# Optimization experiments

Measured on AMD Instinct MI355X. Metric: run time of the kernel, lower is better.

## Reference

```python
import jax, jax.numpy as jnp
import numpy as np

B, S, D = 2, 2048, 1024
H, HD = 16, 64  # num heads, head dim
EPS = 1e-12
SCALING = HD ** -0.5


def rotate_half(x):
    x1, x2 = jnp.split(x, 2, axis=-1)
    return jnp.concatenate([-x2, x1], axis=-1)


def setup_inputs() -> dict:
    key = jax.random.key(0)
    ks = jax.random.split(key, 12)
    hidden_states = jax.random.normal(ks[0], (B, S, D), dtype=jnp.float32)
    # RoPE tables (standard rotate-half convention)
    inv_freq = 1.0 / (10000.0 ** (np.arange(0, HD, 2, dtype=np.float32) / HD))
    pos = np.arange(S, dtype=np.float32)
    freqs = np.outer(pos, inv_freq)  # [S, HD/2]
    emb = np.concatenate([freqs, freqs], axis=-1)  # [S, HD]
    cos = jnp.asarray(np.cos(emb))
    sin = jnp.asarray(np.sin(emb))
    w = 0.02
    return {
        "hidden_states": hidden_states,
        "cos": cos,
        "sin": sin,
        "Wq": jax.random.normal(ks[1], (D, D), dtype=jnp.float32) * w,
        "bq": jnp.zeros((D,), dtype=jnp.float32),
        "Wk": jax.random.normal(ks[2], (D, D), dtype=jnp.float32) * w,
        "bk": jnp.zeros((D,), dtype=jnp.float32),
        "Wv": jax.random.normal(ks[3], (D, D), dtype=jnp.float32) * w,
        "bv": jnp.zeros((D,), dtype=jnp.float32),
        "Wo": jax.random.normal(ks[4], (D, D), dtype=jnp.float32) * w,
        "bo": jnp.zeros((D,), dtype=jnp.float32),
        "ln_w": jnp.ones((D,), dtype=jnp.float32),
        "ln_b": jnp.zeros((D,), dtype=jnp.float32),
    }


def reference(hidden_states, cos, sin, Wq, bq, Wk, bk, Wv, bv, Wo, bo, ln_w, ln_b):
    b, s, d = hidden_states.shape
    # QKV projections -> [b, h, s, hd]
    def proj(W, bias):
        return (hidden_states @ W.T + bias).reshape(b, s, H, HD).transpose(0, 2, 1, 3)
    q, k, v = proj(Wq, bq), proj(Wk, bk), proj(Wv, bv)
    # RoPE (cos/sin broadcast over batch and head dims)
    c = cos[None, None, :, :]
    sn = sin[None, None, :, :]
    q = q * c + rotate_half(q) * sn
    k = k * c + rotate_half(k) * sn
    # Faithful to source: query pre-scaled AND scaling applied inside attention
    q = q * SCALING
    scores = jnp.einsum("bhsd,bhtd->bhst", q, k) * SCALING
    attn = jax.nn.softmax(scores, axis=-1)
    ctx = jnp.einsum("bhst,bhtd->bhsd", attn, v)  # [b,h,s,hd]
    ctx = ctx.transpose(0, 2, 1, 3).reshape(b, s, d)
    # output dense + residual + LayerNorm
    out = ctx @ Wo.T + bo + hidden_states
    mu = jnp.mean(out, axis=-1, keepdims=True)
    var = jnp.var(out, axis=-1, keepdims=True)
    return (out - mu) / jnp.sqrt(var + EPS) * ln_w + ln_b
```

## Files before the change

kernel.cpp:

```cpp
#include <hip/hip_runtime.h>
#include <hip/hip_bf16.h>
#include <stdint.h>


typedef unsigned short ushort_t;
typedef short bf16x8 __attribute__((ext_vector_type(8)));
typedef float f32x4 __attribute__((ext_vector_type(4)));
typedef float f32x16 __attribute__((ext_vector_type(16)));
typedef unsigned short ushort8 __attribute__((ext_vector_type(8)));

#define LOG2E 1.4426950408889634f

__device__ __forceinline__ ushort_t f2b(float f) {
  uint32_t x = __builtin_bit_cast(uint32_t, f);
  return (ushort_t)((x + 0x7FFFu + ((x >> 16) & 1u)) >> 16);
}

__device__ __forceinline__ float b2f(ushort_t u) {
  return __builtin_bit_cast(float, (uint32_t)u << 16);
}

__device__ __forceinline__ uint32_t cvt_pk_bf16(float lo, float hi) {
  uint32_t r;
  asm("v_cvt_pk_bf16_f32 %0, %1, %2" : "=v"(r) : "v"(lo), "v"(hi));
  return r;
}

__device__ __forceinline__ void permswap(uint32_t& a, uint32_t& b) {
  asm volatile("v_permlane32_swap_b32 %0, %1" : "+v"(a), "+v"(b));
}

__device__ __forceinline__ void gload16(const void* gptr, void* ldsptr) {
  __builtin_amdgcn_global_load_lds(
      (const __attribute__((address_space(1))) uint32_t*)gptr,
      (__attribute__((address_space(3))) uint32_t*)ldsptr, 16, 0, 0);
}

__global__ void cast_all_kernel(const float* __restrict__ h,
                                const float* __restrict__ a, const float* __restrict__ b,
                                const float* __restrict__ c, const float* __restrict__ d2,
                                ushort_t* __restrict__ oh, ushort_t* __restrict__ oa,
                                ushort_t* __restrict__ ob, ushort_t* __restrict__ oc,
                                ushort_t* __restrict__ od) {
  const int blk = blockIdx.x;
  const float* src;
  ushort_t* dst;
  int rel;
  if (blk < 2048) { src = h; dst = oh; rel = blk; }
  else {
    const int w = (blk - 2048) >> 9;
    rel = (blk - 2048) & 511;
    src = w == 0 ? a : w == 1 ? b : w == 2 ? c : d2;
    dst = w == 0 ? oa : w == 1 ? ob : w == 2 ? oc : od;
  }
  const int i = (rel * 256 + threadIdx.x) * 8;
  const float4* s = (const float4*)(src + i);
  float4 x = s[0], y = s[1];
  ushort8 o = { f2b(x.x), f2b(x.y), f2b(x.z), f2b(x.w),
                f2b(y.x), f2b(y.y), f2b(y.z), f2b(y.w) };
  *(ushort8*)(dst + i) = o;
}

__global__ __launch_bounds__(256) void gemm_qkv(
    const ushort_t* __restrict__ hid, const ushort_t* __restrict__ wq,
    const ushort_t* __restrict__ wk, const ushort_t* __restrict__ wv,
    const float* __restrict__ bq, const float* __restrict__ bk,
    const float* __restrict__ bv, const float* __restrict__ cosT,
    const float* __restrict__ sinT, ushort_t* __restrict__ qout,
    ushort_t* __restrict__ kout, ushort_t* __restrict__ vtout)
{
  constexpr int K = 1024;
  __shared__ uint4 SB[3072];
  const int which = blockIdx.z;
  const ushort_t* A;
  const ushort_t* Bm;
  const float* bias;
  int m0, n0;
  if (which == 0)      { A = hid; Bm = wq; bias = bq; m0 = blockIdx.x * 128; n0 = blockIdx.y * 128; }
  else if (which == 1) { A = hid; Bm = wk; bias = bk; m0 = blockIdx.x * 128; n0 = blockIdx.y * 128; }
  else                 { A = wv;  Bm = hid; bias = bv; m0 = blockIdx.y * 128; n0 = blockIdx.x * 128; }

  const int tid = threadIdx.x;
  const int wave = tid >> 6, lane = tid & 63;
  const int d = lane & 15, g = lane >> 4;
  const int wm = (wave >> 1) * 64, wn = (wave & 1) * 64;

  const ushort_t* ag = A + (size_t)(m0 + (tid >> 2)) * K + (tid & 3) * 8;
  const ushort_t* bg = Bm + (size_t)(n0 + (tid >> 2)) * K + (tid & 3) * 8;

  f32x4 acc[4][4] = {};

#define STAGE_Q(buf, k0)                                           \
  {                                                                \
    char* dst = (char*)SB + (buf) * 16384 + wave * 1024;           \
    gload16(ag + (k0), dst);                                       \
    gload16(ag + 64 * K + (k0), dst + 4096);                       \
    gload16(bg + (k0), dst + 8192);                                \
    gload16(bg + 64 * K + (k0), dst + 12288);                      \
  }

#define COMPUTE_Q(buf)                                                          \
  {                                                                             \
    bf16x8 af[4], bfr[4];                                                       \
    _Pragma("unroll") for (int i = 0; i < 4; ++i)                               \
        af[i] = __builtin_bit_cast(bf16x8,                                      \
            SB[(buf) * 1024 + (wm + i * 16 + d) * 4 + g]);                      \
    _Pragma("unroll") for (int j = 0; j < 4; ++j)                               \
        bfr[j] = __builtin_bit_cast(bf16x8,                                     \
            SB[(buf) * 1024 + 512 + (wn + j * 16 + d) * 4 + g]);                \
    _Pragma("unroll") for (int i = 0; i < 4; ++i)                               \
        _Pragma("unroll") for (int j = 0; j < 4; ++j)                           \
            acc[i][j] = __builtin_amdgcn_mfma_f32_16x16x32_bf16(                \
                af[i], bfr[j], acc[i][j], 0, 0, 0);                             \
  }

  STAGE_Q(0, 0);
  STAGE_Q(1, 32);
  asm volatile("s_waitcnt vmcnt(4)" ::: "memory");
  __builtin_amdgcn_s_barrier();

  int bufc = 0;
  for (int t = 0; t < 30; ++t) {
    int bufn = bufc + 2; if (bufn >= 3) bufn -= 3;
    STAGE_Q(bufn, (t + 2) * 32);
    COMPUTE_Q(bufc);
    asm volatile("s_waitcnt vmcnt(4)" ::: "memory");
    __builtin_amdgcn_s_barrier();
    bufc = (bufc == 2) ? 0 : bufc + 1;
  }
  COMPUTE_Q(bufc);
  asm volatile("s_waitcnt vmcnt(0)" ::: "memory");
  __builtin_amdgcn_s_barrier();
  bufc = (bufc == 2) ? 0 : bufc + 1;
  COMPUTE_Q(bufc);
#undef STAGE_Q
#undef COMPUTE_Q

  if (which <= 1) {
    ushort_t* O = which == 0 ? qout : kout;
    const float qscale = which == 0 ? (LOG2E / 64.0f) : 1.0f;
    const int head_base = n0 + wn;
    const int h = head_base >> 6;
#pragma unroll
    for (int i = 0; i < 4; ++i) {
#pragma unroll
      for (int r = 0; r < 4; ++r) {
        const int m = m0 + wm + i * 16 + g * 4 + r;
        const int s = m & 2047, b = m >> 11;
#pragma unroll
        for (int j = 0; j < 4; ++j) {
          const int c = j * 16 + d;
          const float v0 = acc[i][j][r] + bias[head_base + c];
          const float v1 = acc[i][j ^ 2][r] + bias[head_base + (c ^ 32)];
          const float rot = (c < 32) ? -v1 : v1;
          const float vr = (v0 * cosT[s * 64 + c] + rot * sinT[s * 64 + c]) * qscale;
          O[(size_t)(((b << 4) + h) * 2048 + s) * 64 + c] = f2b(vr);
        }
      }
    }
  } else {
    ushort_t* O = vtout;
#pragma unroll
    for (int i = 0; i < 4; ++i) {
#pragma unroll
      for (int r = 0; r < 4; ++r) {
        const int fr = m0 + wm + i * 16 + g * 4 + r;
        const float bv2 = bias[fr];
        const int h = fr >> 6, dd = fr & 63;
#pragma unroll
        for (int j = 0; j < 4; ++j) {
          const int tok = n0 + wn + j * 16 + d;
          const int b = tok >> 11, s = tok & 2047;
          O[(size_t)(((b << 4) + h) * 64 + dd) * 2048 + s] = f2b(acc[i][j][r] + bv2);
        }
      }
    }
  }
}

__global__ __launch_bounds__(256) void gemm_wo(
    const ushort_t* __restrict__ A, const ushort_t* __restrict__ B,
    const float* __restrict__ bias, const float* __restrict__ resid,
    ushort_t* __restrict__ O)
{
  constexpr int K = 1024;
  __shared__ uint4 SB[3072];
  const int tid = threadIdx.x;
  const int wave = tid >> 6, lane = tid & 63;
  const int d = lane & 15, g = lane >> 4;
  const int m0 = blockIdx.x * 128, n0 = blockIdx.y * 128;
  const int wm = (wave >> 1) * 64, wn = (wave & 1) * 64;

  const ushort_t* ag = A + (size_t)(m0 + (tid >> 2)) * K + (tid & 3) * 8;
  const ushort_t* bg = B + (size_t)(n0 + (tid >> 2)) * K + (tid & 3) * 8;

  f32x4 acc[4][4] = {};

#define STAGE_W(buf, k0)                                           \
  {                                                                \
    char* dst = (char*)SB + (buf) * 16384 + wave * 1024;           \
    gload16(ag + (k0), dst);                                       \
    gload16(ag + 64 * K + (k0), dst + 4096);                       \
    gload16(bg + (k0), dst + 8192);                                \
    gload16(bg + 64 * K + (k0), dst + 12288);                      \
  }

#define COMPUTE_W(buf)                                                          \
  {                                                                             \
    bf16x8 af[4], bfr[4];                                                       \
    _Pragma("unroll") for (int i = 0; i < 4; ++i)                               \
        af[i] = __builtin_bit_cast(bf16x8,                                      \
            SB[(buf) * 1024 + (wm + i * 16 + d) * 4 + g]);                      \
    _Pragma("unroll") for (int j = 0; j < 4; ++j)                               \
        bfr[j] = __builtin_bit_cast(bf16x8,                                     \
            SB[(buf) * 1024 + 512 + (wn + j * 16 + d) * 4 + g]);                \
    _Pragma("unroll") for (int i = 0; i < 4; ++i)                               \
        _Pragma("unroll") for (int j = 0; j < 4; ++j)                           \
            acc[i][j] = __builtin_amdgcn_mfma_f32_16x16x32_bf16(                \
                af[i], bfr[j], acc[i][j], 0, 0, 0);                             \
  }

  STAGE_W(0, 0);
  STAGE_W(1, 32);
  asm volatile("s_waitcnt vmcnt(4)" ::: "memory");
  __builtin_amdgcn_s_barrier();

  int bufc = 0;
  for (int t = 0; t < 30; ++t) {
    int bufn = bufc + 2; if (bufn >= 3) bufn -= 3;
    STAGE_W(bufn, (t + 2) * 32);
    COMPUTE_W(bufc);
    asm volatile("s_waitcnt vmcnt(4)" ::: "memory");
    __builtin_amdgcn_s_barrier();
    bufc = (bufc == 2) ? 0 : bufc + 1;
  }
  COMPUTE_W(bufc);
  asm volatile("s_waitcnt vmcnt(0)" ::: "memory");
  __builtin_amdgcn_s_barrier();
  bufc = (bufc == 2) ? 0 : bufc + 1;
  COMPUTE_W(bufc);
#undef STAGE_W
#undef COMPUTE_W

#pragma unroll
  for (int i = 0; i < 4; ++i)
#pragma unroll
    for (int r = 0; r < 4; ++r) {
      const int m = m0 + wm + i * 16 + g * 4 + r;
#pragma unroll
      for (int j = 0; j < 4; ++j) {
        const int n = n0 + wn + j * 16 + d;
        O[(size_t)m * 1024 + n] =
            f2b(acc[i][j][r] + bias[n] + resid[(size_t)m * 1024 + n]);
      }
    }
}

__global__ __launch_bounds__(512) void attn_kernel(
    const ushort_t* __restrict__ Q, const ushort_t* __restrict__ Kb,
    const ushort_t* __restrict__ VT, ushort_t* __restrict__ ctx)
{
  __shared__ uint4 KV[2048];
  __shared__ float Ls[256];
  const int orig = blockIdx.x;
  const int wgid = (orig & 7) * 64 + (orig >> 3);
  const int bh = wgid >> 4;
  const int q0 = (wgid & 15) * 128;
  const int tid = threadIdx.x;
  const int wave = tid >> 6, lane = tid & 63;
  const int qw = wave >> 1, half = wave & 1;
  const int ql = lane & 31, h2 = lane >> 5;
  const int qrow = q0 + qw * 32 + ql;

  bf16x8 qf[4];
  {
    const ushort_t* qp = Q + ((size_t)bh * 2048 + qrow) * 64 + h2 * 8;
#pragma unroll
    for (int s = 0; s < 4; ++s)
      qf[s] = __builtin_bit_cast(bf16x8, *(const uint4*)(qp + 16 * s));
  }

  bf16x8 onesf;
  {
    uint4 ou = {0x3F803F80u, 0x3F803F80u, 0x3F803F80u, 0x3F803F80u};
    onesf = __builtin_bit_cast(bf16x8, ou);
  }

  const int st_row = tid >> 3, st_c8 = tid & 7;
  const ushort_t* kgp = Kb + (size_t)(bh * 2048 + st_row) * 64 + st_c8 * 8;
  const ushort_t* vgp = VT + (size_t)(bh * 64 + st_row) * 2048 + st_c8 * 8;
  const int sidx = st_row * 8 + (st_c8 ^ (st_row & 7));

  uint4 kr = *(const uint4*)(kgp);
  uint4 vr = *(const uint4*)(vgp);
  KV[sidx] = kr;
  KV[512 + sidx] = vr;
  __syncthreads();

  f32x16 cacc[2] = {};
  f32x16 lacc = {};

#define ATT_COMPUTE(CB)                                                         \
  {                                                                             \
    f32x16 z = {};                                                              \
    _Pragma("unroll") for (int s = 0; s < 4; ++s) {                             \
      bf16x8 kf = __builtin_bit_cast(bf16x8,                                    \
          KV[(CB) + (half * 32 + ql) * 8 + ((2 * s + h2) ^ (ql & 7))]);         \
      z = __builtin_amdgcn_mfma_f32_32x32x16_bf16(kf, qf[s], z, 0, 0, 0);       \
    }                                                                           \
    bf16x8 pf[2];                                                               \
    _Pragma("unroll") for (int s2 = 0; s2 < 2; ++s2) {                          \
      const int rb = s2 * 8;                                                    \
      float p0 = __builtin_amdgcn_exp2f(z[rb + 0]);                             \
      float p1 = __builtin_amdgcn_exp2f(z[rb + 1]);                             \
      float p2 = __builtin_amdgcn_exp2f(z[rb + 2]);                             \
      float p3 = __builtin_amdgcn_exp2f(z[rb + 3]);                             \
      float p4 = __builtin_amdgcn_exp2f(z[rb + 4]);                             \
      float p5 = __builtin_amdgcn_exp2f(z[rb + 5]);                             \
      float p6 = __builtin_amdgcn_exp2f(z[rb + 6]);                             \
      float p7 = __builtin_amdgcn_exp2f(z[rb + 7]);                             \
      uint32_t a1 = cvt_pk_bf16(p0, p1);                                        \
      uint32_t a2 = cvt_pk_bf16(p2, p3);                                        \
      uint32_t b1 = cvt_pk_bf16(p4, p5);                                        \
      uint32_t b2 = cvt_pk_bf16(p6, p7);                                        \
      permswap(a1, b1);                                                         \
      permswap(a2, b2);                                                         \
      uint4 u = {a1, a2, b1, b2};                                               \
      pf[s2] = __builtin_bit_cast(bf16x8, u);                                   \
    }                                                                           \
    _Pragma("unroll") for (int s2 = 0; s2 < 2; ++s2)                            \
      lacc = __builtin_amdgcn_mfma_f32_32x32x16_bf16(onesf, pf[s2], lacc,       \
                                                     0, 0, 0);                  \
    _Pragma("unroll") for (int dt = 0; dt < 2; ++dt)                            \
      _Pragma("unroll") for (int s2 = 0; s2 < 2; ++s2) {                        \
        const int s = 2 * half + s2;                                            \
        bf16x8 vf = __builtin_bit_cast(bf16x8,                                  \
            KV[(CB) + 512 + (dt * 32 + ql) * 8 + ((2 * s + h2) ^ (ql & 7))]);   \
        cacc[dt] = __builtin_amdgcn_mfma_f32_32x32x16_bf16(vf, pf[s2],          \
                                                           cacc[dt], 0, 0, 0); \
      }                                                                         \
  }

  const ushort_t* kP = kgp + 4096;
  const ushort_t* vP = vgp + 64;
  for (int tt = 0; tt < 16; ++tt) {
    kr = *(const uint4*)(kP);
    vr = *(const uint4*)(vP);
    ATT_COMPUTE(0)
    KV[1024 + sidx] = kr;
    KV[1536 + sidx] = vr;
    __syncthreads();
    if (tt < 15) {
      kr = *(const uint4*)(kP + 4096);
      vr = *(const uint4*)(vP + 64);
    }
    ATT_COMPUTE(1024)
    if (tt < 15) {
      KV[sidx] = kr;
      KV[512 + sidx] = vr;
      __syncthreads();
    }
    kP += 8192;
    vP += 128;
  }
#undef ATT_COMPUTE

  float lsum = lacc[0];

  __syncthreads();
  float* Lf = (float*)KV;
  const int slot = qw * 64 + lane;
  if (half == 1) {
#pragma unroll
    for (int dt = 0; dt < 2; ++dt)
#pragma unroll
      for (int r = 0; r < 16; ++r)
        Lf[slot * 32 + ((dt * 16 + r) ^ (lane & 31))] = cacc[dt][r];
    Ls[slot] = lsum;
  }
  __syncthreads();
  if (half == 0) {
#pragma unroll
    for (int dt = 0; dt < 2; ++dt)
#pragma unroll
      for (int r = 0; r < 16; ++r)
        cacc[dt][r] += Lf[slot * 32 + ((dt * 16 + r) ^ (lane & 31))];
    lsum += Ls[slot];

    const float rinv = 1.0f / lsum;
    const int b = bh >> 4, h = bh & 15;
    ushort_t* cp = ctx + ((size_t)(b * 2048 + qrow)) * 1024 + h * 64 + h2 * 4;
#pragma unroll
    for (int dt = 0; dt < 2; ++dt)
#pragma unroll
      for (int t = 0; t < 4; ++t) {
        uint2 w;
        w.x = cvt_pk_bf16(cacc[dt][4 * t + 0] * rinv, cacc[dt][4 * t + 1] * rinv);
        w.y = cvt_pk_bf16(cacc[dt][4 * t + 2] * rinv, cacc[dt][4 * t + 3] * rinv);
        *(uint2*)(cp + dt * 32 + t * 8) = w;
      }
  }
}

__global__ __launch_bounds__(256) void ln_kernel(const ushort_t* __restrict__ x,
    const float* __restrict__ w, const float* __restrict__ b2, float* __restrict__ out)
{
  const int row = blockIdx.x, tid = threadIdx.x;
  const uint2 u = ((const uint2*)(x + (size_t)row * 1024))[tid];
  float v0 = b2f((ushort_t)(u.x & 0xFFFF));
  float v1 = b2f((ushort_t)(u.x >> 16));
  float v2 = b2f((ushort_t)(u.y & 0xFFFF));
  float v3 = b2f((ushort_t)(u.y >> 16));
  float s = (v0 + v1) + (v2 + v3);
  float ss = (v0 * v0 + v1 * v1) + (v2 * v2 + v3 * v3);
#pragma unroll
  for (int off = 32; off > 0; off >>= 1) {
    s += __shfl_down(s, off, 64);
    ss += __shfl_down(ss, off, 64);
  }
  __shared__ float red[8];
  if ((tid & 63) == 0) { red[tid >> 6] = s; red[4 + (tid >> 6)] = ss; }
  __syncthreads();
  const float S = red[0] + red[1] + red[2] + red[3];
  const float SS = red[4] + red[5] + red[6] + red[7];
  const float mu = S * (1.f / 1024.f);
  const float rstd = rsqrtf(SS * (1.f / 1024.f) - mu * mu + 1e-12f);
  const int c = tid * 4;
  float4 o;
  o.x = (v0 - mu) * rstd * w[c + 0] + b2[c + 0];
  o.y = (v1 - mu) * rstd * w[c + 1] + b2[c + 1];
  o.z = (v2 - mu) * rstd * w[c + 2] + b2[c + 2];
  o.w = (v3 - mu) * rstd * w[c + 3] + b2[c + 3];
  ((float4*)(out + (size_t)row * 1024))[tid] = o;
}

extern "C" void kernel_launch(void* const* d_in, const int* in_sizes, int n_in,
                              void* d_out, int out_size, void* d_ws, size_t ws_size,
                              hipStream_t stream) {
  const float* hidden = (const float*)d_in[0];
  const float* cosT = (const float*)d_in[1];
  const float* sinT = (const float*)d_in[2];
  const float* Wq = (const float*)d_in[3];
  const float* bq = (const float*)d_in[4];
  const float* Wk = (const float*)d_in[5];
  const float* bk = (const float*)d_in[6];
  const float* Wv = (const float*)d_in[7];
  const float* bv = (const float*)d_in[8];
  const float* Wo = (const float*)d_in[9];
  const float* bo = (const float*)d_in[10];
  const float* lnw = (const float*)d_in[11];
  const float* lnb = (const float*)d_in[12];

  char* ws = (char*)d_ws;
  const size_t MB = 1u << 20;
  ushort_t* hid_bf = (ushort_t*)(ws);
  ushort_t* wq_bf = (ushort_t*)(ws + 8 * MB);
  ushort_t* wk_bf = (ushort_t*)(ws + 10 * MB);
  ushort_t* wv_bf = (ushort_t*)(ws + 12 * MB);
  ushort_t* wo_bf = (ushort_t*)(ws + 14 * MB);
  ushort_t* q_buf = (ushort_t*)(ws + 16 * MB);
  ushort_t* k_buf = (ushort_t*)(ws + 24 * MB);
  ushort_t* vt_buf = (ushort_t*)(ws + 32 * MB);
  ushort_t* ctx_bf = (ushort_t*)(ws + 40 * MB);
  ushort_t* out_pre = (ushort_t*)(ws + 16 * MB);

  cast_all_kernel<<<4096, 256, 0, stream>>>(hidden, Wq, Wk, Wv, Wo,
                                            hid_bf, wq_bf, wk_bf, wv_bf, wo_bf);

  gemm_qkv<<<dim3(32, 8, 3), 256, 0, stream>>>(hid_bf, wq_bf, wk_bf, wv_bf,
                                               bq, bk, bv, cosT, sinT,
                                               q_buf, k_buf, vt_buf);
  attn_kernel<<<512, 512, 0, stream>>>(q_buf, k_buf, vt_buf, ctx_bf);
  gemm_wo<<<dim3(32, 8), 256, 0, stream>>>(ctx_bf, wo_bf, bo, hidden, out_pre);
  ln_kernel<<<4096, 256, 0, stream>>>(out_pre, lnw, lnb, (float*)d_out);
}
```

Baseline: 108.2 us.

## Fuse Q and K projections in one block to share the hidden-state tile

Q/K blocks now load one hidden-state tile and multiply it against both Wq and Wk, keeping two accumulator sets. V keeps its own block path, and the grid shrinks from three z-slices to two. The goal is fewer global loads of the activations and shared RoPE table reads. The cost is more registers and LDS per block (72KB), which may cut occupancy, and uneven work between Q/K blocks and V blocks.

```diff
diff --git a/kernel.cpp b/kernel.cpp
--- a/kernel.cpp
+++ b/kernel.cpp
@@ -70,108 +70,169 @@
     ushort_t* __restrict__ kout, ushort_t* __restrict__ vtout)
 {
   constexpr int K = 1024;
-  __shared__ uint4 SB[3072];
-  const int which = blockIdx.z;
-  const ushort_t* A;
-  const ushort_t* Bm;
-  const float* bias;
-  int m0, n0;
-  if (which == 0)      { A = hid; Bm = wq; bias = bq; m0 = blockIdx.x * 128; n0 = blockIdx.y * 128; }
-  else if (which == 1) { A = hid; Bm = wk; bias = bk; m0 = blockIdx.x * 128; n0 = blockIdx.y * 128; }
-  else                 { A = wv;  Bm = hid; bias = bv; m0 = blockIdx.y * 128; n0 = blockIdx.x * 128; }
-
+  __shared__ uint4 SB[4608];
   const int tid = threadIdx.x;
   const int wave = tid >> 6, lane = tid & 63;
   const int d = lane & 15, g = lane >> 4;
   const int wm = (wave >> 1) * 64, wn = (wave & 1) * 64;
 
-  const ushort_t* ag = A + (size_t)(m0 + (tid >> 2)) * K + (tid & 3) * 8;
-  const ushort_t* bg = Bm + (size_t)(n0 + (tid >> 2)) * K + (tid & 3) * 8;
-
-  f32x4 acc[4][4] = {};
-
-#define STAGE_Q(buf, k0)                                           \
+  if (blockIdx.z == 0) {
+    const int m0 = blockIdx.x * 128, n0 = blockIdx.y * 128;
+    const ushort_t* ag = hid + (size_t)(m0 + (tid >> 2)) * K + (tid & 3) * 8;
+    const ushort_t* qg = wq + (size_t)(n0 + (tid >> 2)) * K + (tid & 3) * 8;
+    const ushort_t* kg = wk + (size_t)(n0 + (tid >> 2)) * K + (tid & 3) * 8;
+
+    f32x4 accq[4][4] = {};
+    f32x4 acck[4][4] = {};
+
+#define STAGE_QK(buf, k0)                                          \
   {                                                                \
-    char* dst = (char*)SB + (buf) * 16384 + wave * 1024;           \
-    gload16(ag + (k0), dst);                                       \
-    gload16(ag + 64 * K + (k0), dst + 4096);                       \
-    gload16(bg + (k0), dst + 8192);                                \
-    gload16(bg + 64 * K + (k0), dst + 12288);                      \
-  }
-
-#define COMPUTE_Q(buf)                                                          \
+    char* base = (char*)(SB + (buf) * 1536) + wave * 1024;         \
+    gload16(ag + (k0), base);                                      \
+    gload16(ag + 64 * K + (k0), base + 4096);                      \
+    gload16(qg + (k0), base + 8192);                               \
+    gload16(qg + 64 * K + (k0), base + 12288);                     \
+    gload16(kg + (k0), base + 16384);                              \
+    gload16(kg + 64 * K + (k0), base + 20480);                     \
+  }
+
+#define COMPUTE_QK(buf)                                                         \
+  {                                                                             \
+    bf16x8 af[4], bfq[4], bfk[4];                                               \
+    _Pragma("unroll") for (int i = 0; i < 4; ++i)                               \
+        af[i] = __builtin_bit_cast(bf16x8,                                      \
+            SB[(buf) * 1536 + (wm + i * 16 + d) * 4 + g]);                      \
+    _Pragma("unroll") for (int j = 0; j < 4; ++j) {                             \
+        bfq[j] = __builtin_bit_cast(bf16x8,                                     \
+            SB[(buf) * 1536 + 512 + (wn + j * 16 + d) * 4 + g]);                \
+        bfk[j] = __builtin_bit_cast(bf16x8,                                     \
+            SB[(buf) * 1536 + 1024 + (wn + j * 16 + d) * 4 + g]);               \
+    }                                                                           \
+    _Pragma("unroll") for (int i = 0; i < 4; ++i)                               \
+        _Pragma("unroll") for (int j = 0; j < 4; ++j) {                         \
+            accq[i][j] = __builtin_amdgcn_mfma_f32_16x16x32_bf16(               \
+                af[i], bfq[j], accq[i][j], 0, 0, 0);                            \
+            acck[i][j] = __builtin_amdgcn_mfma_f32_16x16x32_bf16(               \
+                af[i], bfk[j], acck[i][j], 0, 0, 0);                            \
+        }                                                                       \
+  }
+
+    STAGE_QK(0, 0);
+    STAGE_QK(1, 32);
+    asm volatile("s_waitcnt vmcnt(6)" ::: "memory");
+    __builtin_amdgcn_s_barrier();
+
+    int bufc = 0;
+    for (int t = 0; t < 30; ++t) {
+      int bufn = bufc + 2; if (bufn >= 3) bufn -= 3;
+      STAGE_QK(bufn, (t + 2) * 32);
+      COMPUTE_QK(bufc);
+      asm volatile("s_waitcnt vmcnt(6)" ::: "memory");
+      __builtin_amdgcn_s_barrier();
+      bufc = (bufc == 2) ? 0 : bufc + 1;
+    }
+    COMPUTE_QK(bufc);
+    asm volatile("s_waitcnt vmcnt(0)" ::: "memory");
+    __builtin_amdgcn_s_barrier();
+    bufc = (bufc == 2) ? 0 : bufc + 1;
+    COMPUTE_QK(bufc);
+#undef STAGE_QK
+#undef COMPUTE_QK
+
+    const int head_base = n0 + wn;
+    const int h = head_base >> 6;
+#pragma unroll
+    for (int i = 0; i < 4; ++i) {
+#pragma unroll
+      for (int r = 0; r < 4; ++r) {
+        const int m = m0 + wm + i * 16 + g * 4 + r;
+        const int s = m & 2047, b = m >> 11;
+        const size_t orow = (size_t)(((b << 4) + h) * 2048 + s) * 64;
+#pragma unroll
+        for (int j = 0; j < 4; ++j) {
+          const int c = j * 16 + d;
+          const float cs = cosT[s * 64 + c];
+          const float sn = sinT[s * 64 + c];
+          {
+            const float v0 = accq[i][j][r] + bq[head_base + c];
+            const float v1 = accq[i][j ^ 2][r] + bq[head_base + (c ^ 32)];
+            const float rot = (c < 32) ? -v1 : v1;
+            qout[orow + c] = f2b((v0 * cs + rot * sn) * (LOG2E / 64.0f));
+          }
+          {
+            const float v0 = acck[i][j][r] + bk[head_base + c];
+            const float v1 = acck[i][j ^ 2][r] + bk[head_base + (c ^ 32)];
+            const float rot = (c < 32) ? -v1 : v1;
+            kout[orow + c] = f2b(v0 * cs + rot * sn);
+          }
+        }
+      }
+    }
+  } else {
+    const int m0 = blockIdx.y * 128, n0 = blockIdx.x * 128;
+    const ushort_t* ag = wv + (size_t)(m0 + (tid >> 2)) * K + (tid & 3) * 8;
+    const ushort_t* bg = hid + (size_t)(n0 + (tid >> 2)) * K + (tid & 3) * 8;
+
+    f32x4 acc[4][4] = {};
+
+#define STAGE_V(buf, k0)                                           \
+  {                                                                \
+    char* base = (char*)(SB + (buf) * 1536) + wave * 1024;         \
+    gload16(ag + (k0), base);                                      \
+    gload16(ag + 64 * K + (k0), base + 4096);                      \
+    gload16(bg + (k0), base + 8192);                               \
+    gload16(bg + 64 * K + (k0), base + 12288);                     \
+  }
+
+#define COMPUTE_V(buf)                                                          \
   {                                                                             \
     bf16x8 af[4], bfr[4];                                                       \
     _Pragma("unroll") for (int i = 0; i < 4; ++i)                               \
         af[i] = __builtin_bit_cast(bf16x8,                                      \
-            SB[(buf) * 1024 + (wm + i * 16 + d) * 4 + g]);                      \
+            SB[(buf) * 1536 + (wm + i * 16 + d) * 4 + g]);                      \
     _Pragma("unroll") for (int j = 0; j < 4; ++j)                               \
         bfr[j] = __builtin_bit_cast(bf16x8,                                     \
-            SB[(buf) * 1024 + 512 + (wn + j * 16 + d) * 4 + g]);                \
+            SB[(buf) * 1536 + 512 + (wn + j * 16 + d) * 4 + g]);                \
     _Pragma("unroll") for (int i = 0; i < 4; ++i)                               \
         _Pragma("unroll") for (int j = 0; j < 4; ++j)                           \
             acc[i][j] = __builtin_amdgcn_mfma_f32_16x16x32_bf16(                \
                 af[i], bfr[j], acc[i][j], 0, 0, 0);                             \
   }
 
-  STAGE_Q(0, 0);
-  STAGE_Q(1, 32);
-  asm volatile("s_waitcnt vmcnt(4)" ::: "memory");
-  __builtin_amdgcn_s_barrier();
-
-  int bufc = 0;
-  for (int t = 0; t < 30; ++t) {
-    int bufn = bufc + 2; if (bufn >= 3) bufn -= 3;
-    STAGE_Q(bufn, (t + 2) * 32);
-    COMPUTE_Q(bufc);
+    STAGE_V(0, 0);
+    STAGE_V(1, 32);
     asm volatile("s_waitcnt vmcnt(4)" ::: "memory");
     __builtin_amdgcn_s_barrier();
+
+    int bufc = 0;
+    for (int t = 0; t < 30; ++t) {
+      int bufn = bufc + 2; if (bufn >= 3) bufn -= 3;
+      STAGE_V(bufn, (t + 2) * 32);
+      COMPUTE_V(bufc);
+      asm volatile("s_waitcnt vmcnt(4)" ::: "memory");
+      __builtin_amdgcn_s_barrier();
+      bufc = (bufc == 2) ? 0 : bufc + 1;
+    }
+    COMPUTE_V(bufc);
+    asm volatile("s_waitcnt vmcnt(0)" ::: "memory");
+    __builtin_amdgcn_s_barrier();
     bufc = (bufc == 2) ? 0 : bufc + 1;
-  }
-  COMPUTE_Q(bufc);
-  asm volatile("s_waitcnt vmcnt(0)" ::: "memory");
-  __builtin_amdgcn_s_barrier();
-  bufc = (bufc == 2) ? 0 : bufc + 1;
-  COMPUTE_Q(bufc);
-#undef STAGE_Q
-#undef COMPUTE_Q
-
-  if (which <= 1) {
-    ushort_t* O = which == 0 ? qout : kout;
-    const float qscale = which == 0 ? (LOG2E / 64.0f) : 1.0f;
-    const int head_base = n0 + wn;
-    const int h = head_base >> 6;
-#pragma unroll
-    for (int i = 0; i < 4; ++i) {
-#pragma unroll
-      for (int r = 0; r < 4; ++r) {
-        const int m = m0 + wm + i * 16 + g * 4 + r;
-        const int s = m & 2047, b = m >> 11;
-#pragma unroll
-        for (int j = 0; j < 4; ++j) {
-          const int c = j * 16 + d;
-          const float v0 = acc[i][j][r] + bias[head_base + c];
-          const float v1 = acc[i][j ^ 2][r] + bias[head_base + (c ^ 32)];
-          const float rot = (c < 32) ? -v1 : v1;
-          const float vr = (v0 * cosT[s * 64 + c] + rot * sinT[s * 64 + c]) * qscale;
-          O[(size_t)(((b << 4) + h) * 2048 + s) * 64 + c] = f2b(vr);
-        }
-      }
-    }
-  } else {
-    ushort_t* O = vtout;
+    COMPUTE_V(bufc);
+#undef STAGE_V
+#undef COMPUTE_V
+
 #pragma unroll
     for (int i = 0; i < 4; ++i) {
 #pragma unroll
       for (int r = 0; r < 4; ++r) {
         const int fr = m0 + wm + i * 16 + g * 4 + r;
-        const float bv2 = bias[fr];
+        const float bv2 = bv[fr];
         const int h = fr >> 6, dd = fr & 63;
 #pragma unroll
         for (int j = 0; j < 4; ++j) {
           const int tok = n0 + wn + j * 16 + d;
           const int b = tok >> 11, s = tok & 2047;
-          O[(size_t)(((b << 4) + h) * 64 + dd) * 2048 + s] = f2b(acc[i][j][r] + bv2);
+          vtout[(size_t)(((b << 4) + h) * 64 + dd) * 2048 + s] = f2b(acc[i][j][r] + bv2);
         }
       }
     }
@@ -467,7 +528,7 @@
   cast_all_kernel<<<4096, 256, 0, stream>>>(hidden, Wq, Wk, Wv, Wo,
                                             hid_bf, wq_bf, wk_bf, wv_bf, wo_bf);
 
-  gemm_qkv<<<dim3(32, 8, 3), 256, 0, stream>>>(hid_bf, wq_bf, wk_bf, wv_bf,
+  gemm_qkv<<<dim3(32, 8, 2), 256, 0, stream>>>(hid_bf, wq_bf, wk_bf, wv_bf,
                                                bq, bk, bv, cosT, sinT,
                                                q_buf, k_buf, vt_buf);
   attn_kernel<<<512, 512, 0, stream>>>(q_buf, k_buf, vt_buf, ctx_bf);
```

Result: slower. 117.4 us (+8.5%).
